# Optimization experiments

Hardware: AMD Instinct MI355X
Metric: run time of the kernel (lower is better)

The kernel has to match this reference:

```python
import jax, jax.numpy as jnp
import numpy as np
import math

MAXL = 2; C = 16; A = 32; B = 2; LAYERS = 2; CUT = 0.5


def _cg_coeff(l1, l2, l, m1, m2, m):
    if m1 + m2 != m or l < abs(l1 - l2) or l > l1 + l2:
        return 0.0
    f = math.factorial
    pre = math.sqrt((2 * l + 1) * f(l + l1 - l2) * f(l - l1 + l2) * f(l1 + l2 - l) / f(l1 + l2 + l + 1))
    pre *= math.sqrt(f(l + m) * f(l - m) * f(l1 + m1) * f(l1 - m1) * f(l2 + m2) * f(l2 - m2))
    s = 0.0
    for k in range(0, l1 + l2 + 1):
        d = (k, l1 + l2 - l - k, l1 - m1 - k, l2 + m2 - k, l - l2 + m1 + k, l - l1 - m2 + k)
        if min(d) < 0:
            continue
        s += (-1.0) ** k / (f(d[0]) * f(d[1]) * f(d[2]) * f(d[3]) * f(d[4]) * f(d[5]))
    return pre * s


def _cg_matrix(l1, l2, l):
    M = np.zeros((2 * l1 + 1, 2 * l2 + 1, 2 * l + 1), dtype=np.float32)
    for m1 in range(-l1, l1 + 1):
        for m2 in range(-l2, l2 + 1):
            m = m1 + m2
            if -l <= m <= l:
                M[m1 + l1, m2 + l2, m + l] = _cg_coeff(l1, l2, l, m1, m2, m)
    return M

_CG = {}
for _l1 in range(MAXL + 1):
    for _l2 in range(MAXL + 1):
        for _l in range(abs(_l1 - _l2), min(_l1 + _l2, MAXL) + 1):
            _CG[(_l1, _l2, _l)] = jnp.asarray(_cg_matrix(_l1, _l2, _l))


def _cg_product(parts1, parts2):
    # GElib-style CG product: channel dim is the outer product of input channels,
    # concatenated over valid (l1,l2) couplings in loop order.
    out = [[] for _ in range(MAXL + 1)]
    for l1, p1 in enumerate(parts1):
        for l2, p2 in enumerate(parts2):
            for l in range(abs(l1 - l2), min(l1 + l2, MAXL) + 1):
                t = jnp.einsum('xyz,...xc,...yd->...zcd', _CG[(l1, l2, l)], p1, p2)
                out[l].append(t.reshape(t.shape[:-2] + (t.shape[-2] * t.shape[-1],)))
    return [jnp.concatenate(o, axis=-1) for o in out]


def _sph(rel_pos):
    # Real spherical harmonics (orthonormal convention) of the normalized rel vector,
    # broadcast across the C channels of type_sph.
    eps = 1e-6
    r = jnp.sqrt(jnp.sum(rel_pos * rel_pos, axis=-1, keepdims=True) + eps)
    u = rel_pos / r
    x, y, z = u[..., 0], u[..., 1], u[..., 2]
    Y0 = 0.28209479 * jnp.ones_like(x)[..., None]
    Y1 = 0.48860251 * jnp.stack([y, z, x], axis=-1)
    Y2 = jnp.stack([1.09254843 * x * y, 1.09254843 * y * z,
                    0.31539157 * (3.0 * z * z - 1.0), 1.09254843 * x * z,
                    0.54627422 * (x * x - y * y)], axis=-1)
    return [jnp.repeat(Y[..., None], C, axis=-1) for Y in (Y0, Y1, Y2)]


def _cg_layer(parts, conn, sph, wnl, wrel):
    # message pass: masked neighbor sum (Rmask1 gather)
    mp = [jnp.einsum('bij,bjomc->biomc', conn, p) for p in parts]
    cg_nl = _cg_product(mp, mp)
    mixed_nl = [jnp.einsum('baomt,aotc->baomc', p, w) for p, w in zip(cg_nl, wnl)]
    rep = [jnp.tile(p, (1, 1, A, 1, 1)) for p in mixed_nl]  # adims [A,1] -> [A,A]
    cg_rel = _cg_product(rep, sph)
    mixed_rel = [jnp.einsum('bijmt,ijtc->bijmc', p, w) for p, w in zip(cg_rel, wrel)]
    return [jnp.sum(p, axis=2, keepdims=True) for p in mixed_rel]


def _scalars(parts):
    b, a = parts[0].shape[0], parts[0].shape[1]
    s0 = parts[0].reshape(b, a, C)
    sn = [jnp.einsum('baomc,baomd->bacd', p, p).reshape(b, a, C * C) for p in parts]
    return jnp.concatenate([s0] + sn, axis=-1)


def setup_inputs() -> dict:
    key = jax.random.key(0)
    ks = jax.random.split(key, 20)
    tau_nl = [3 * C * C, 6 * C * C, 6 * C * C]
    inp = {
        'v0': jax.random.normal(ks[0], (B, A, 1, 1, C), jnp.float32),
        'v1': jax.random.normal(ks[1], (B, A, 1, 3, C), jnp.float32),
        'v2': jax.random.normal(ks[2], (B, A, 1, 5, C), jnp.float32),
        'rel_pos': jax.random.normal(ks[3], (B, A, A, 3), jnp.float32),
        'norms': jax.random.uniform(ks[4], (B, A, A), jnp.float32),
    }
    i = 5
    for layer in range(LAYERS):
        for l in range(MAXL + 1):
            inp['wnl%d_%d' % (layer, l)] = 0.02 * jax.random.normal(ks[i], (A, 1, tau_nl[l], C), jnp.float32); i += 1
            inp['wrel%d_%d' % (layer, l)] = 0.02 * jax.random.normal(ks[i], (A, A, tau_nl[l], C), jnp.float32); i += 1
    return inp


def reference(v0, v1, v2, rel_pos, norms,
              wnl0_0, wrel0_0, wnl0_1, wrel0_1, wnl0_2, wrel0_2,
              wnl1_0, wrel1_0, wnl1_1, wrel1_1, wnl1_2, wrel1_2):
    parts = [v0, v1, v2]
    sph = _sph(rel_pos)
    conn = (norms < CUT).astype(v0.dtype)
    wnl = [[wnl0_0, wnl0_1, wnl0_2], [wnl1_0, wnl1_1, wnl1_2]]
    wrel = [[wrel0_0, wrel0_1, wrel0_2], [wrel1_0, wrel1_1, wrel1_2]]
    outs = []
    for L in range(LAYERS):
        parts = _cg_layer(parts, conn, sph, wnl[L], wrel[L])
        outs.append(_scalars(parts))
    return jnp.concatenate(outs, axis=0)
```

## Files before the change

### kernel.cpp

```cpp
#include <hip/hip_runtime.h>

#define NA 32
#define NB 2
#define NC 16

constexpr int KL1[15]   = {0,1,2, 0,1,1,1,2,2, 0,1,1,2,2,2};
constexpr int KL2[15]   = {0,1,2, 1,0,1,2,1,2, 2,1,2,0,1,2};
constexpr int KOFF[15]  = {0,1,10, 35,44,53,80,125,170, 245,270,315,390,415,490};
constexpr int KLBASE[3] = {0,3,9};
constexpr int KLOFF[3]  = {0,1,4};
constexpr int KOFF3[3]  = {0,1024,4096};
__constant__ int CP_L1[15]   = {0,1,2, 0,1,1,1,2,2, 0,1,1,2,2,2};
__constant__ int CP_L2[15]   = {0,1,2, 1,0,1,2,1,2, 2,1,2,0,1,2};
__constant__ int CP_OFF[15]  = {0,1,10, 35,44,53,80,125,170, 245,270,315,390,415,490};
__constant__ int LBASE[3] = {0,3,9};
__constant__ int LOFF[3]  = {0,1,4};
__constant__ int OFF3[3]  = {0,1024,4096};

constexpr double cfact(int n){ double r=1.0; for(int i=2;i<=n;++i) r*=(double)i; return r; }
constexpr double csqrt(double x){
    double g = (x > 1.0) ? x : 1.0, prev = 0.0;
    for (int i = 0; i < 60 && g != prev; ++i) { prev = g; g = 0.5*(g + x/g); }
    return g;
}
struct CGT { float v[616]; };
constexpr CGT build_cg() {
    CGT t{};
    for (int cp=0; cp<15; ++cp){
        int l1=KL1[cp], l2=KL2[cp];
        int l = (cp<3)?0:((cp<9)?1:2);
        int n1=2*l1+1, n2=2*l2+1, nl=2*l+1;
        for (int x=0;x<n1;++x) for(int y=0;y<n2;++y) for(int z=0;z<nl;++z){
            int m1=x-l1, m2=y-l2, m=z-l;
            double val=0.0;
            if (m1+m2==m){
                double pre = csqrt((2.0*l+1.0)*cfact(l+l1-l2)*cfact(l-l1+l2)*cfact(l1+l2-l)/cfact(l1+l2+l+1));
                pre *= csqrt(cfact(l+m)*cfact(l-m)*cfact(l1+m1)*cfact(l1-m1)*cfact(l2+m2)*cfact(l2-m2));
                double s=0.0;
                for(int k=0;k<=l1+l2;++k){
                    int d0=k,d1=l1+l2-l-k,d2=l1-m1-k,d3=l2+m2-k,d4=l-l2+m1+k,d5=l-l1-m2+k;
                    if(d0<0||d1<0||d2<0||d3<0||d4<0||d5<0) continue;
                    double term = 1.0/(cfact(d0)*cfact(d1)*cfact(d2)*cfact(d3)*cfact(d4)*cfact(d5));
                    s += (k & 1) ? -term : term;
                }
                val = pre*s;
            }
            t.v[KOFF[cp] + (x*n2+y)*nl + z] = (float)val;
        }
    }
    return t;
}
__constant__ CGT CGC = build_cg();

template<int L>
__device__ void nl_body(int i, int b, int z,
    const float* __restrict__ p0, const float* __restrict__ p1, const float* __restrict__ p2,
    const float* __restrict__ norms, const float* __restrict__ wnl,
    float* __restrict__ mnl, float* smem)
{
    constexpr int MD  = 2*L+1;
    constexpr int TAU = (L == 0) ? 768 : 1536;
    constexpr int NK  = TAU / 256;

    float* shCG = smem;
    float* mp   = smem + 616;
    float* shcg = mp + 144;
    float* red  = shcg + TAU;

    const int tid = threadIdx.x;
    const int wave = tid >> 6, lane = tid & 63;

    for (int e = tid; e < 616; e += 256) shCG[e] = CGC.v[e];

    if (tid < 144) {
        int xt = tid >> 4, c = tid & 15;
        int lp = (xt < 1) ? 0 : ((xt < 4) ? 1 : 2);
        int x = xt - KLOFF[lp];
        int md = 2*lp+1;
        const float* pp = (lp == 0) ? p0 : ((lp == 1) ? p1 : p2);
        const float* nr = norms + (b*NA + i)*NA;
        float s = 0.0f;
        for (int j = 0; j < NA; ++j) {
            if (nr[j] < 0.5f) s += pp[((b*NA + j)*md + x)*NC + c];
        }
        mp[tid] = s;
    }
    __syncthreads();

    {
        const int c = tid >> 4, d = tid & 15;
#pragma unroll
        for (int k = 0; k < NK; ++k) {
            const int cp = KLBASE[L] + k;
            const int l1 = KL1[cp], l2 = KL2[cp];
            const int n1 = 2*l1+1, n2 = 2*l2+1;
            float s = 0.0f;
#pragma unroll
            for (int x = 0; x < n1; ++x) {
                float mv = mp[(KLOFF[l1] + x)*NC + c];
#pragma unroll
                for (int y = 0; y < n2; ++y)
                    s += shCG[KOFF[cp] + (x*n2 + y)*MD + z] * mv * mp[(KLOFF[l2] + y)*NC + d];
            }
            shcg[k*256 + tid] = s;
        }
    }
    __syncthreads();

    {
        const int tg = tid >> 4, cidx = tid & 15;
        float s = 0.0f;
        for (int ss = 0; ss < TAU/16; ++ss) {
            int t = tg + (ss << 4);
            s += shcg[t] * wnl[(i*TAU + t)*NC + cidx];
        }
        s += __shfl_xor(s, 16);
        s += __shfl_xor(s, 32);
        if (lane < 16) red[wave*16 + lane] = s;
    }
    __syncthreads();
    if (tid < 16) {
        float s = red[tid] + red[16 + tid] + red[32 + tid] + red[48 + tid];
        mnl[KOFF3[L] + ((b*NA + i)*MD + z)*NC + tid] = s;
    }
}

__device__ void scal_body(int b, int a, const float* __restrict__ pin,
                          float* __restrict__ out, float* sp)
{
    const int tid = threadIdx.x;
    for (int e = tid; e < 9*NC; e += 256) {
        int xt = e / NC, c = e % NC;
        int lp = (xt < 1) ? 0 : ((xt < 4) ? 1 : 2);
        sp[e] = pin[OFF3[lp] + ((b*NA + a)*(2*lp+1) + (xt - LOFF[lp]))*NC + c];
    }
    __syncthreads();
    float* orow = out + (size_t)(b*NA + a)*784;
    for (int e = tid; e < 784; e += 256) {
        float v;
        if (e < 16) {
            v = sp[e];
        } else {
            int g = e - 16;
            int lb = g >> 8; int c = (g >> 4) & 15; int d = g & 15;
            int md = 2*lb+1;
            float s = 0.0f;
            for (int zz = 0; zz < md; ++zz)
                s += sp[(LOFF[lb] + zz)*NC + c] * sp[(LOFF[lb] + zz)*NC + d];
            v = s;
        }
        orow[e] = v;
    }
}

__global__ __launch_bounds__(256) void k_nl(
    const float* __restrict__ p0, const float* __restrict__ p1, const float* __restrict__ p2,
    const float* __restrict__ norms,
    const float* __restrict__ w0, const float* __restrict__ w1, const float* __restrict__ w2,
    float* __restrict__ mnl, float* __restrict__ po,
    const float* __restrict__ prev_po, float* __restrict__ prev_out)
{
    __shared__ __align__(16) float smem[2360];
    const int bx = blockIdx.x;
    if (bx >= 576) {
        if (prev_po) {
            int sidx = bx - 576;
            scal_body(sidx >> 5, sidx & 31, prev_po, prev_out, smem);
        }
        return;
    }
    if (threadIdx.x < 16) po[bx*16 + threadIdx.x] = 0.0f;

    const int lq = bx >> 5, i = bx & 31;
    if (lq < 2)      nl_body<0>(i, lq, 0, p0, p1, p2, norms, w0, mnl, smem);
    else if (lq < 8) { int g = lq - 2; nl_body<1>(i, g/3, g%3, p0, p1, p2, norms, w1, mnl, smem); }
    else             { int g = lq - 8; nl_body<2>(i, g/5, g%5, p0, p1, p2, norms, w2, mnl, smem); }
}

template<int L>
__device__ void rel_body(int i, int jq, int half,
    const float* __restrict__ wr, const float* __restrict__ mnl,
    const float* __restrict__ relpos, float* __restrict__ pout,
    float* smem)
{
    constexpr int MD  = 2*L+1;
    constexpr int NBZ = 2*MD;
    constexpr int TAU = (L==0) ? 768 : 1536;

    float*  shCG = smem;
    float*  shY  = smem + 616;
    float*  shM  = shY + 72;
    float*  shG  = shM + 288;
    float4* shR  = (float4*)(shG + 4*48*NBZ);

    const int tid = threadIdx.x;
    const int wave = tid >> 6, lane = tid & 63;

    for (int e = tid; e < 616; e += 256) shCG[e] = CGC.v[e];

    if (tid < 8) {
        int jj = tid >> 1, b = tid & 1;
        int j = (jq << 2) + jj;
        const float* rp = relpos + (((size_t)(b*NA + i))*NA + j)*3;
        float px = rp[0], py = rp[1], pz = rp[2];
        float rr = sqrtf(px*px + py*py + pz*pz + 1e-6f);
        float ux = px/rr, uy = py/rr, uz = pz/rr;
        float* Y = shY + tid*9;
        Y[0] = 0.28209479f;
        Y[1] = 0.48860251f*uy; Y[2] = 0.48860251f*uz; Y[3] = 0.48860251f*ux;
        Y[4] = 1.09254843f*ux*uy; Y[5] = 1.09254843f*uy*uz;
        Y[6] = 0.31539157f*(3.0f*uz*uz - 1.0f);
        Y[7] = 1.09254843f*ux*uz; Y[8] = 0.54627422f*(ux*ux - uy*uy);
    }
    for (int e = tid; e < NB*9*NC; e += 256) {
        int b = e / (9*NC); int rem = e % (9*NC);
        int xt = rem / NC;  int c = rem % NC;
        int lp = (xt < 1) ? 0 : ((xt < 4) ? 1 : 2);
        shM[e] = mnl[OFF3[lp] + ((b*NA + i)*(2*lp+1) + (xt - LOFF[lp]))*NC + c];
    }
    __syncthreads();

    for (int e = tid; e < 4*48*NBZ; e += 256) {
        int q = e % NBZ; int r = (e/NBZ) % 48; int jj = e / (NBZ*48);
        int b = q / MD, z = q % MD;
        int R = half*48 + r; int k = R >> 4, c = R & 15;
        int cp = LBASE[L] + k;
        int l1 = CP_L1[cp], l2 = CP_L2[cp];
        int n1 = 2*l1+1, n2 = 2*l2+1;
        const float* cgp = shCG + CP_OFF[cp];
        float s = 0.0f;
        for (int x = 0; x < n1; ++x) {
            float mv = shM[(b*9 + LOFF[l1] + x)*NC + c];
            for (int y = 0; y < n2; ++y)
                s += cgp[(x*n2 + y)*MD + z] * mv * shY[((jj<<1)+b)*9 + LOFF[l2] + y];
        }
        shG[e] = s;
    }
    __syncthreads();

    const float* wbase = wr + ((size_t)(i*NA + (jq<<2))*TAU + half*(TAU/2))*16;

    float4 acc[NBZ];
#pragma unroll
    for (int q = 0; q < NBZ; ++q) acc[q] = make_float4(0.f,0.f,0.f,0.f);

    for (int jj = 0; jj < 4; ++jj) {
        const float* bb = wbase + (size_t)jj*TAU*16;
        const float* gbase = shG + jj*48*NBZ + wave*NBZ;
#pragma unroll 4
        for (int ch = 0; ch < 12; ++ch) {
            const float4 v = *(const float4*)(bb + ch*1024 + tid*4);
            const float* gp = gbase + ch*4*NBZ;
#pragma unroll
            for (int q = 0; q < NBZ; ++q) {
                float g = gp[q];
                acc[q].x += g*v.x; acc[q].y += g*v.y; acc[q].z += g*v.z; acc[q].w += g*v.w;
            }
        }
    }

#pragma unroll
    for (int q = 0; q < NBZ; ++q) {
        float4 v = acc[q];
#pragma unroll
        for (int m = 4; m <= 32; m <<= 1) {
            v.x += __shfl_xor(v.x, m); v.y += __shfl_xor(v.y, m);
            v.z += __shfl_xor(v.z, m); v.w += __shfl_xor(v.w, m);
        }
        acc[q] = v;
    }
    if (lane < 4) {
#pragma unroll
        for (int q = 0; q < NBZ; ++q) shR[(wave*4 + lane)*NBZ + q] = acc[q];
    }
    __syncthreads();
    for (int e = tid; e < NBZ*16; e += 256) {
        int q = e >> 4, cp = e & 15, qq = cp >> 2, cc = cp & 3;
        float s = 0.0f;
        for (int w = 0; w < 4; ++w) {
            const float* pr = (const float*)&shR[(w*4 + qq)*NBZ + q];
            s += pr[cc];
        }
        int b = q / MD, z = q % MD;
        atomicAdd(&pout[OFF3[L] + ((b*NA + i)*MD + z)*NC + cp], s);
    }
}

__global__ __launch_bounds__(256, 4) void k_rel(
    const float* __restrict__ mnl, const float* __restrict__ relpos,
    const float* __restrict__ wr0, const float* __restrict__ wr1, const float* __restrict__ wr2,
    float* __restrict__ pout)
{
    __shared__ __align__(16) float smem[3536];
    const int bx = blockIdx.x;
    const int s = bx >> 8, idx = bx & 255;
    const int i = idx >> 3, jq = idx & 7;
    if (s == 0)      rel_body<0>(i, jq, 0, wr0, mnl, relpos, pout, smem);
    else if (s == 1) rel_body<1>(i, jq, 0, wr1, mnl, relpos, pout, smem);
    else if (s == 2) rel_body<1>(i, jq, 1, wr1, mnl, relpos, pout, smem);
    else if (s == 3) rel_body<2>(i, jq, 0, wr2, mnl, relpos, pout, smem);
    else             rel_body<2>(i, jq, 1, wr2, mnl, relpos, pout, smem);
}

__global__ __launch_bounds__(256) void k_scal(const float* __restrict__ pin, float* __restrict__ out)
{
    __shared__ float sp[9*NC];
    scal_body(blockIdx.x >> 5, blockIdx.x & 31, pin, out, sp);
}

extern "C" void kernel_launch(void* const* d_in, const int* in_sizes, int n_in,
                              void* d_out, int out_size, void* d_ws, size_t ws_size,
                              hipStream_t stream)
{
    const float* v0     = (const float*)d_in[0];
    const float* v1     = (const float*)d_in[1];
    const float* v2     = (const float*)d_in[2];
    const float* relpos = (const float*)d_in[3];
    const float* norms  = (const float*)d_in[4];
    const float* wnl[2][3] = {
        {(const float*)d_in[5],  (const float*)d_in[7],  (const float*)d_in[9]},
        {(const float*)d_in[11], (const float*)d_in[13], (const float*)d_in[15]}};
    const float* wrel[2][3] = {
        {(const float*)d_in[6],  (const float*)d_in[8],  (const float*)d_in[10]},
        {(const float*)d_in[12], (const float*)d_in[14], (const float*)d_in[16]}};

    float* ws  = (float*)d_ws;
    float* mnl = ws;
    float* pA  = ws + 9216;
    float* pB  = ws + 18432;
    float* out = (float*)d_out;

    k_nl<<<640, 256, 0, stream>>>(v0, v1, v2, norms,
                                  wnl[0][0], wnl[0][1], wnl[0][2], mnl, pA,
                                  nullptr, nullptr);
    k_rel<<<1280, 256, 0, stream>>>(mnl, relpos, wrel[0][0], wrel[0][1], wrel[0][2], pA);
    k_nl<<<640, 256, 0, stream>>>(pA, pA + 1024, pA + 4096, norms,
                                  wnl[1][0], wnl[1][1], wnl[1][2], mnl, pB,
                                  pA, out);
    k_rel<<<1280, 256, 0, stream>>>(mnl, relpos, wrel[1][0], wrel[1][1], wrel[1][2], pB);
    k_scal<<<64, 256, 0, stream>>>(pB, out + (size_t)NB * NA * 784);
}
```

Before: 541.5 us.

## Prefetch rel weights into register ring, vectorize nl weight reduction

The rel kernel's weight streaming loop is fully unrolled over all 48 chunks and uses a P-deep register ring of float4 prefetches, so global loads are issued ahead of the FMAs that use them. The nl kernel's weight dot product switches from scalar loads to float4 loads with a shuffle-then-shared-memory reduction, and the masked neighbor sum becomes branchless and unrolled. The launch bound for k_rel is raised to 5 blocks per SM. The extra prefetch registers together with the tighter occupancy bound risk spills or lower occupancy.

New measurement: 496.5 us. 1.09x faster.

```diff
diff --git a/kernel.cpp b/kernel.cpp
--- a/kernel.cpp
+++ b/kernel.cpp
@@ -80,8 +80,10 @@
         const float* pp = (lp == 0) ? p0 : ((lp == 1) ? p1 : p2);
         const float* nr = norms + (b*NA + i)*NA;
         float s = 0.0f;
+#pragma unroll
         for (int j = 0; j < NA; ++j) {
-            if (nr[j] < 0.5f) s += pp[((b*NA + j)*md + x)*NC + c];
+            float msk = (nr[j] < 0.5f) ? 1.0f : 0.0f;
+            s += msk * pp[((b*NA + j)*md + x)*NC + c];
         }
         mp[tid] = s;
     }
@@ -108,19 +110,34 @@
     __syncthreads();
 
     {
-        const int tg = tid >> 4, cidx = tid & 15;
+        constexpr int PER = TAU / 4;
+        constexpr int IT  = PER / 16;
+        const int t_low = lane >> 2, c4 = lane & 3;
+        const float4* w4 = (const float4*)(wnl + (size_t)i * TAU * 16);
+        float4 acc = make_float4(0.f, 0.f, 0.f, 0.f);
+        const int tb = wave * PER + t_low;
+#pragma unroll 4
+        for (int it = 0; it < IT; ++it) {
+            int t = tb + it * 16;
+            float sc = shcg[t];
+            float4 wv = w4[t * 4 + c4];
+            acc.x += sc * wv.x; acc.y += sc * wv.y; acc.z += sc * wv.z; acc.w += sc * wv.w;
+        }
+#pragma unroll
+        for (int m = 4; m <= 32; m <<= 1) {
+            acc.x += __shfl_xor(acc.x, m); acc.y += __shfl_xor(acc.y, m);
+            acc.z += __shfl_xor(acc.z, m); acc.w += __shfl_xor(acc.w, m);
+        }
+        float4* red4 = (float4*)red;
+        if (lane < 4) red4[wave * 4 + lane] = acc;
+    }
+    __syncthreads();
+    if (tid < 16) {
+        const float4* red4 = (const float4*)red;
+        int c4 = tid >> 2, comp = tid & 3;
         float s = 0.0f;
-        for (int ss = 0; ss < TAU/16; ++ss) {
-            int t = tg + (ss << 4);
-            s += shcg[t] * wnl[(i*TAU + t)*NC + cidx];
-        }
-        s += __shfl_xor(s, 16);
-        s += __shfl_xor(s, 32);
-        if (lane < 16) red[wave*16 + lane] = s;
-    }
-    __syncthreads();
-    if (tid < 16) {
-        float s = red[tid] + red[16 + tid] + red[32 + tid] + red[48 + tid];
+#pragma unroll
+        for (int w = 0; w < 4; ++w) s += ((const float*)&red4[w * 4 + c4])[comp];
         mnl[KOFF3[L] + ((b*NA + i)*MD + z)*NC + tid] = s;
     }
 }
@@ -186,6 +203,7 @@
     constexpr int MD  = 2*L+1;
     constexpr int NBZ = 2*MD;
     constexpr int TAU = (L==0) ? 768 : 1536;
+    constexpr int P   = (L==2) ? 5 : 8;
 
     float*  shCG = smem;
     float*  shY  = smem + 616;
@@ -239,23 +257,31 @@
     __syncthreads();
 
     const float* wbase = wr + ((size_t)(i*NA + (jq<<2))*TAU + half*(TAU/2))*16;
+    const float* tb = wbase + tid*4;
+
+    float4 buf[P];
+#pragma unroll
+    for (int c = 0; c < P; ++c)
+        buf[c] = *(const float4*)(tb + (size_t)(c/12)*TAU*16 + (c%12)*1024);
 
     float4 acc[NBZ];
 #pragma unroll
     for (int q = 0; q < NBZ; ++q) acc[q] = make_float4(0.f,0.f,0.f,0.f);
 
-    for (int jj = 0; jj < 4; ++jj) {
-        const float* bb = wbase + (size_t)jj*TAU*16;
-        const float* gbase = shG + jj*48*NBZ + wave*NBZ;
-#pragma unroll 4
-        for (int ch = 0; ch < 12; ++ch) {
-            const float4 v = *(const float4*)(bb + ch*1024 + tid*4);
-            const float* gp = gbase + ch*4*NBZ;
-#pragma unroll
-            for (int q = 0; q < NBZ; ++q) {
-                float g = gp[q];
-                acc[q].x += g*v.x; acc[q].y += g*v.y; acc[q].z += g*v.z; acc[q].w += g*v.w;
-            }
+#pragma unroll
+    for (int c = 0; c < 48; ++c) {
+        const float4 v = buf[c % P];
+        if (c + P < 48)
+            buf[c % P] = *(const float4*)(tb + (size_t)((c+P)/12)*TAU*16 + ((c+P)%12)*1024);
+        const int jj = c/12, r = (c%12)*4 + wave;
+        const float* gp = shG + (jj*48 + r)*NBZ;
+        float g[NBZ];
+#pragma unroll
+        for (int q = 0; q < NBZ; ++q) g[q] = gp[q];
+#pragma unroll
+        for (int q = 0; q < NBZ; ++q) {
+            acc[q].x += g[q]*v.x; acc[q].y += g[q]*v.y;
+            acc[q].z += g[q]*v.z; acc[q].w += g[q]*v.w;
         }
     }
 
@@ -286,7 +312,7 @@
     }
 }
 
-__global__ __launch_bounds__(256, 4) void k_rel(
+__global__ __launch_bounds__(256, 5) void k_rel(
     const float* __restrict__ mnl, const float* __restrict__ relpos,
     const float* __restrict__ wr0, const float* __restrict__ wr1, const float* __restrict__ wr2,
     float* __restrict__ pout)
```
